# Performance work log

Hardware: AMD Instinct MI355X
Metric: run time of the kernel (lower is better)

The kernel has to match this reference:

```python
import jax, jax.numpy as jnp
import numpy as np

BLOCK_NUM = 64
B, M, K, N = 4, 4096, 4096, 4096  # batch, rows, in_features, out_features


def setup_inputs() -> dict:
    key = jax.random.key(0)
    k1, k2 = jax.random.split(key)
    x = jax.random.normal(k1, (B, M, K), dtype=jnp.float32)
    weight = jax.random.normal(k2, (K, N), dtype=jnp.float32) * 0.02
    return {"x": x, "weight": weight}


def reference(x, weight):
    # Block-local matmul: output block (i, j) = A_block(i, j) @ W_block(i, j).
    # No cross-block reduction: each (i, j) output block depends on exactly one
    # A block and one W block. Vectorized as a single einsum over all blocks.
    b, m, k = x.shape
    k2, n = weight.shape
    Bn = BLOCK_NUM
    r, c, o = m // Bn, k // Bn, n // Bn  # per-block rows / contract / cols
    A = x.reshape(b, Bn, r, Bn, c)        # [b, i, r, j, c]
    W = weight.reshape(Bn, c, Bn, o)      # [i, c, j, o] (rows split by i, cols by j)
    out = jnp.einsum('birjc,icjo->birjo', A, W)
    return out.reshape(b, m, n)
```

## Files before the change

### kernel.cpp

```cpp
#include <hip/hip_runtime.h>
#include <hip/hip_bf16.h>


typedef short bf16x8 __attribute__((ext_vector_type(8)));
typedef float f32x4 __attribute__((ext_vector_type(4)));

__device__ __forceinline__ unsigned short f2bf(float f) {
    union { float f; unsigned int u; } v; v.f = f;
    unsigned int u = v.u;
    u += 0x7fffu + ((u >> 16) & 1u);
    return (unsigned short)(u >> 16);
}

__global__ __launch_bounds__(256, 4) void block_matmul_kernel(
    const float* __restrict__ x, const float* __restrict__ w,
    float* __restrict__ out) {
    __shared__ unsigned short As[64 * 64];
    __shared__ unsigned short Ws[64 * 64];

    const int nwg   = 4 * 64 * 64;
    const int chunk = nwg >> 3;
    int orig = blockIdx.x;
    int wg   = (orig & 7) * chunk + (orig >> 3);

    int b  = wg & 3;
    int ij = wg >> 2;
    int i  = ij >> 6;
    int j  = ij & 63;

    const float* Ab = x   + ((size_t)b * 4096 + (size_t)i * 64) * 4096 + (size_t)j * 64;
    const float* Wb = w   + ((size_t)i * 64) * 4096 + (size_t)j * 64;
    float*       Ob = out + ((size_t)b * 4096 + (size_t)i * 64) * 4096 + (size_t)j * 64;

    const int t = threadIdx.x;

    #pragma unroll
    for (int it = 0; it < 4; ++it) {
        int idx = it * 256 + t;
        int m   = idx >> 4;
        int k4  = (idx & 15) << 2;
        float4 v = *reinterpret_cast<const float4*>(Ab + (size_t)m * 4096 + k4);
        unsigned long long pk =
            (unsigned long long)f2bf(v.x)        |
            ((unsigned long long)f2bf(v.y) << 16) |
            ((unsigned long long)f2bf(v.z) << 32) |
            ((unsigned long long)f2bf(v.w) << 48);
        int addr = m * 128 + ((k4 * 2) ^ ((m & 7) << 4));
        *reinterpret_cast<unsigned long long*>(reinterpret_cast<char*>(As) + addr) = pk;
    }

    {
        int n  = t & 63;
        int kq = (t >> 6) << 2;
        #pragma unroll
        for (int it = 0; it < 4; ++it) {
            int kb = it * 16 + kq;
            float f0 = Wb[(size_t)(kb + 0) * 4096 + n];
            float f1 = Wb[(size_t)(kb + 1) * 4096 + n];
            float f2 = Wb[(size_t)(kb + 2) * 4096 + n];
            float f3 = Wb[(size_t)(kb + 3) * 4096 + n];
            unsigned long long pk =
                (unsigned long long)f2bf(f0)        |
                ((unsigned long long)f2bf(f1) << 16) |
                ((unsigned long long)f2bf(f2) << 32) |
                ((unsigned long long)f2bf(f3) << 48);
            int addr = n * 128 + ((kb * 2) ^ ((n & 7) << 4));
            *reinterpret_cast<unsigned long long*>(reinterpret_cast<char*>(Ws) + addr) = pk;
        }
    }

    __syncthreads();

    const int l  = t & 63;
    const int wv = t >> 6;
    const int lr = l & 15;
    const int lk = l >> 4;

    f32x4 acc[4] = {{0.f,0.f,0.f,0.f},{0.f,0.f,0.f,0.f},
                    {0.f,0.f,0.f,0.f},{0.f,0.f,0.f,0.f}};

    #pragma unroll
    for (int kt = 0; kt < 2; ++kt) {
        int kbyte = kt * 64 + lk * 16;
        int am = wv * 16 + lr;
        bf16x8 af = *reinterpret_cast<const bf16x8*>(
            reinterpret_cast<const char*>(As) + am * 128 + (kbyte ^ ((am & 7) << 4)));
        #pragma unroll
        for (int nt = 0; nt < 4; ++nt) {
            int bn = nt * 16 + lr;
            bf16x8 bfr = *reinterpret_cast<const bf16x8*>(
                reinterpret_cast<const char*>(Ws) + bn * 128 + (kbyte ^ ((bn & 7) << 4)));
            acc[nt] = __builtin_amdgcn_mfma_f32_16x16x32_bf16(af, bfr, acc[nt], 0, 0, 0);
        }
    }

    #pragma unroll
    for (int nt = 0; nt < 4; ++nt) {
        #pragma unroll
        for (int r = 0; r < 4; ++r) {
            int orow = wv * 16 + lk * 4 + r;
            int ocol = nt * 16 + lr;
            Ob[(size_t)orow * 4096 + ocol] = acc[nt][r];
        }
    }
}

extern "C" void kernel_launch(void* const* d_in, const int* in_sizes, int n_in,
                              void* d_out, int out_size, void* d_ws, size_t ws_size,
                              hipStream_t stream) {
    const float* x = (const float*)d_in[0];
    const float* w = (const float*)d_in[1];
    float* out = (float*)d_out;

    dim3 grid(4 * 64 * 64);
    dim3 block(256);
    block_matmul_kernel<<<grid, block, 0, stream>>>(x, w, out);
}
```

Before: 143.5 us.

## Reuse weight block across batch and pipeline A loads via global_load_lds

Each workgroup now handles one (i,j) block for all four batches: it loads and converts the weight block once, then streams the fp32 A tiles for each batch straight into LDS with global_load_lds, double-buffered with explicit vmcnt waits so the next batch's load overlaps the current MFMA and store. The grid shrinks by a factor of four. This removes the repeated weight loads and the register round trip for A, at the cost of more LDS per workgroup and hand-tuned vmcnt counts that must match the outstanding loads and stores exactly.

New measurement: 148.6 us. 1.04x slower.

```diff
diff --git a/kernel.cpp b/kernel.cpp
--- a/kernel.cpp
+++ b/kernel.cpp
@@ -12,97 +12,127 @@
     return (unsigned short)(u >> 16);
 }
 
+__device__ __forceinline__ bf16x8 pack8(float4 a, float4 b) {
+    bf16x8 r;
+    r[0] = (short)f2bf(a.x); r[1] = (short)f2bf(a.y);
+    r[2] = (short)f2bf(a.z); r[3] = (short)f2bf(a.w);
+    r[4] = (short)f2bf(b.x); r[5] = (short)f2bf(b.y);
+    r[6] = (short)f2bf(b.z); r[7] = (short)f2bf(b.w);
+    return r;
+}
+
+#define BBYTES 67108864ull
+#define BELEMS 16777216ull
+
+#define WAITV(N) do { asm volatile("s_waitcnt vmcnt(" #N ")" ::: "memory"); \
+                      __builtin_amdgcn_sched_barrier(0); } while (0)
+
 __global__ __launch_bounds__(256, 4) void block_matmul_kernel(
     const float* __restrict__ x, const float* __restrict__ w,
     float* __restrict__ out) {
-    __shared__ unsigned short As[64 * 64];
-    __shared__ unsigned short Ws[64 * 64];
+    __shared__ char smem[40960];
 
-    const int nwg   = 4 * 64 * 64;
-    const int chunk = nwg >> 3;
+    const int t   = threadIdx.x;
+    const int l   = t & 63;
+    const int wv  = t >> 6;
+    const int lr  = l & 15;
+    const int lhi = l >> 4;
+
     int orig = blockIdx.x;
-    int wg   = (orig & 7) * chunk + (orig >> 3);
+    int wg   = (orig & 7) * 512 + (orig >> 3);
+    int i = wg >> 6;
+    int j = wg & 63;
 
-    int b  = wg & 3;
-    int ij = wg >> 2;
-    int i  = ij >> 6;
-    int j  = ij & 63;
+    const size_t rowbase = (size_t)i * 64;
+    const size_t colbase = (size_t)j * 64;
 
-    const float* Ab = x   + ((size_t)b * 4096 + (size_t)i * 64) * 4096 + (size_t)j * 64;
-    const float* Wb = w   + ((size_t)i * 64) * 4096 + (size_t)j * 64;
-    float*       Ob = out + ((size_t)b * 4096 + (size_t)i * 64) * 4096 + (size_t)j * 64;
-
-    const int t = threadIdx.x;
-
+    const float* Wb = w + rowbase * 4096 + colbase;
+    const int wn = t & 63;
+    const int cg = t >> 6;
+    float wreg[16];
+    #pragma unroll
+    for (int it = 0; it < 4; ++it)
+        #pragma unroll
+        for (int r = 0; r < 4; ++r)
+            wreg[it * 4 + r] = Wb[(size_t)(cg * 16 + it * 4 + r) * 4096 + wn];
     #pragma unroll
     for (int it = 0; it < 4; ++it) {
-        int idx = it * 256 + t;
-        int m   = idx >> 4;
-        int k4  = (idx & 15) << 2;
-        float4 v = *reinterpret_cast<const float4*>(Ab + (size_t)m * 4096 + k4);
+        int cc = (cg * 16 + it * 4) * 2;
         unsigned long long pk =
-            (unsigned long long)f2bf(v.x)        |
-            ((unsigned long long)f2bf(v.y) << 16) |
-            ((unsigned long long)f2bf(v.z) << 32) |
-            ((unsigned long long)f2bf(v.w) << 48);
-        int addr = m * 128 + ((k4 * 2) ^ ((m & 7) << 4));
-        *reinterpret_cast<unsigned long long*>(reinterpret_cast<char*>(As) + addr) = pk;
+            (unsigned long long)f2bf(wreg[it * 4 + 0])         |
+            ((unsigned long long)f2bf(wreg[it * 4 + 1]) << 16) |
+            ((unsigned long long)f2bf(wreg[it * 4 + 2]) << 32) |
+            ((unsigned long long)f2bf(wreg[it * 4 + 3]) << 48);
+        *reinterpret_cast<unsigned long long*>(
+            smem + wn * 128 + (cc ^ ((wn & 7) << 4))) = pk;
+    }
+    __syncthreads();
+
+    const char* Axbase = (const char*)x +
+        ((rowbase + wv * 16) * 4096 + colbase) * 4;
+    const int c16 = (l & 15) * 16;
+
+#define DMA(b_, p_) {                                                         \
+    _Pragma("unroll") for (int s = 0; s < 4; ++s) {                           \
+        int rl   = s * 4 + lhi;                                               \
+        int csrc = c16 ^ ((rl & 7) << 4);                                     \
+        const char* gp = Axbase + (size_t)(b_) * BBYTES +                     \
+                         (size_t)rl * 16384 + csrc;                           \
+        char* lp = smem + 8192 + (p_) * 16384 + wv * 4096 + s * 1024;         \
+        __builtin_amdgcn_global_load_lds(                                     \
+            (const __attribute__((address_space(1))) void*)gp,                \
+            (__attribute__((address_space(3))) void*)lp, 16, 0, 0);           \
+    } }
+
+    char* Alane = smem + 8192 + wv * 4096 + lr * 256;
+    const int fsw = (lr & 7) << 4;
+
+    DMA(0, 0);
+    DMA(1, 1);
+
+#define BATCH(b_, p_, NW, NEXT, HASNEXT) {                                    \
+    WAITV(NW);                                                                \
+    const char* Ab = Alane + (p_) * 16384;                                    \
+    float4 f00 = *reinterpret_cast<const float4*>(                            \
+        Ab + ((lhi * 32) ^ fsw));                                             \
+    float4 f01 = *reinterpret_cast<const float4*>(                            \
+        Ab + ((lhi * 32 + 16) ^ fsw));                                        \
+    float4 f10 = *reinterpret_cast<const float4*>(                            \
+        Ab + ((128 + lhi * 32) ^ fsw));                                       \
+    float4 f11 = *reinterpret_cast<const float4*>(                            \
+        Ab + ((128 + lhi * 32 + 16) ^ fsw));                                  \
+    bf16x8 af0 = pack8(f00, f01);                                             \
+    bf16x8 af1 = pack8(f10, f11);                                             \
+    __builtin_amdgcn_sched_barrier(0);                                        \
+    if (HASNEXT) DMA(NEXT, p_);                                               \
+    f32x4 acc[4];                                                             \
+    _Pragma("unroll") for (int nt = 0; nt < 4; ++nt)                          \
+        acc[nt] = (f32x4){0.f, 0.f, 0.f, 0.f};                                \
+    _Pragma("unroll") for (int nt = 0; nt < 4; ++nt) {                        \
+        int bn = nt * 16 + lr;                                                \
+        bf16x8 w0 = *reinterpret_cast<const bf16x8*>(                         \
+            smem + bn * 128 + ((lhi * 16) ^ ((bn & 7) << 4)));                \
+        acc[nt] = __builtin_amdgcn_mfma_f32_16x16x32_bf16(                    \
+            af0, w0, acc[nt], 0, 0, 0);                                       \
+    }                                                                         \
+    _Pragma("unroll") for (int nt = 0; nt < 4; ++nt) {                        \
+        int bn = nt * 16 + lr;                                                \
+        bf16x8 w1 = *reinterpret_cast<const bf16x8*>(                         \
+            smem + bn * 128 + ((64 + lhi * 16) ^ ((bn & 7) << 4)));           \
+        acc[nt] = __builtin_amdgcn_mfma_f32_16x16x32_bf16(                    \
+            af1, w1, acc[nt], 0, 0, 0);                                       \
+    }                                                                         \
+    float* Ob = out + (size_t)(b_) * BELEMS +                                 \
+                (rowbase + wv * 16) * 4096 + colbase;                         \
+    _Pragma("unroll") for (int nt = 0; nt < 4; ++nt)                          \
+    _Pragma("unroll") for (int r = 0; r < 4; ++r)                             \
+        Ob[(size_t)(lhi * 4 + r) * 4096 + nt * 16 + lr] = acc[nt][r];         \
     }
 
-    {
-        int n  = t & 63;
-        int kq = (t >> 6) << 2;
-        #pragma unroll
-        for (int it = 0; it < 4; ++it) {
-            int kb = it * 16 + kq;
-            float f0 = Wb[(size_t)(kb + 0) * 4096 + n];
-            float f1 = Wb[(size_t)(kb + 1) * 4096 + n];
-            float f2 = Wb[(size_t)(kb + 2) * 4096 + n];
-            float f3 = Wb[(size_t)(kb + 3) * 4096 + n];
-            unsigned long long pk =
-                (unsigned long long)f2bf(f0)        |
-                ((unsigned long long)f2bf(f1) << 16) |
-                ((unsigned long long)f2bf(f2) << 32) |
-                ((unsigned long long)f2bf(f3) << 48);
-            int addr = n * 128 + ((kb * 2) ^ ((n & 7) << 4));
-            *reinterpret_cast<unsigned long long*>(reinterpret_cast<char*>(Ws) + addr) = pk;
-        }
-    }
-
-    __syncthreads();
-
-    const int l  = t & 63;
-    const int wv = t >> 6;
-    const int lr = l & 15;
-    const int lk = l >> 4;
-
-    f32x4 acc[4] = {{0.f,0.f,0.f,0.f},{0.f,0.f,0.f,0.f},
-                    {0.f,0.f,0.f,0.f},{0.f,0.f,0.f,0.f}};
-
-    #pragma unroll
-    for (int kt = 0; kt < 2; ++kt) {
-        int kbyte = kt * 64 + lk * 16;
-        int am = wv * 16 + lr;
-        bf16x8 af = *reinterpret_cast<const bf16x8*>(
-            reinterpret_cast<const char*>(As) + am * 128 + (kbyte ^ ((am & 7) << 4)));
-        #pragma unroll
-        for (int nt = 0; nt < 4; ++nt) {
-            int bn = nt * 16 + lr;
-            bf16x8 bfr = *reinterpret_cast<const bf16x8*>(
-                reinterpret_cast<const char*>(Ws) + bn * 128 + (kbyte ^ ((bn & 7) << 4)));
-            acc[nt] = __builtin_amdgcn_mfma_f32_16x16x32_bf16(af, bfr, acc[nt], 0, 0, 0);
-        }
-    }
-
-    #pragma unroll
-    for (int nt = 0; nt < 4; ++nt) {
-        #pragma unroll
-        for (int r = 0; r < 4; ++r) {
-            int orow = wv * 16 + lk * 4 + r;
-            int ocol = nt * 16 + lr;
-            Ob[(size_t)orow * 4096 + ocol] = acc[nt][r];
-        }
-    }
+    BATCH(0, 0, 4,  2, 1);
+    BATCH(1, 1, 20, 3, 1);
+    BATCH(2, 0, 36, 0, 0);
+    BATCH(3, 1, 32, 0, 0);
 }
 
 extern "C" void kernel_launch(void* const* d_in, const int* in_sizes, int n_in,
@@ -112,7 +142,7 @@
     const float* w = (const float*)d_in[1];
     float* out = (float*)d_out;
 
-    dim3 grid(4 * 64 * 64);
+    dim3 grid(4096);
     dim3 block(256);
     block_matmul_kernel<<<grid, block, 0, stream>>>(x, w, out);
 }
```

## Process four adjacent blocks per workgroup with wide coalesced loads and LDS-staged stores

Applied to the files above, without the earlier changes.

Each workgroup now handles a 64x256 strip (four neighbouring j blocks) instead of one 64x64 block, cutting the grid from 16384 to 4096 workgroups. All global loads are issued up front into registers as full-row 1 KB coalesced float4 reads before the bf16 conversion. The output is staged through LDS with a swizzle so each row is written with wide float4 stores instead of scattered scalar stores. The trade-off is 64 KB of LDS, higher register use, and a lower occupancy target of 2 blocks per SIMD instead of 4, which may reduce latency hiding for this memory-bound kernel.

New measurement: 128.3 us. -10.6%, faster.

```diff
diff --git a/kernel.cpp b/kernel.cpp
--- a/kernel.cpp
+++ b/kernel.cpp
@@ -12,96 +12,135 @@
     return (unsigned short)(u >> 16);
 }
 
-__global__ __launch_bounds__(256, 4) void block_matmul_kernel(
+__device__ __forceinline__ unsigned long long pack4(float4 v) {
+    return  (unsigned long long)f2bf(v.x)        |
+           ((unsigned long long)f2bf(v.y) << 16) |
+           ((unsigned long long)f2bf(v.z) << 32) |
+           ((unsigned long long)f2bf(v.w) << 48);
+}
+
+__device__ __forceinline__ unsigned long long pack4s(float a, float b,
+                                                     float c, float d) {
+    return  (unsigned long long)f2bf(a)        |
+           ((unsigned long long)f2bf(b) << 16) |
+           ((unsigned long long)f2bf(c) << 32) |
+           ((unsigned long long)f2bf(d) << 48);
+}
+
+#define BELEMS 16777216ull
+
+#define FENCE() asm volatile("s_waitcnt lgkmcnt(0)" ::: "memory")
+
+__global__ __launch_bounds__(256, 2) void block_matmul_kernel(
     const float* __restrict__ x, const float* __restrict__ w,
     float* __restrict__ out) {
-    __shared__ unsigned short As[64 * 64];
-    __shared__ unsigned short Ws[64 * 64];
+    __shared__ char smem[65536];
 
-    const int nwg   = 4 * 64 * 64;
-    const int chunk = nwg >> 3;
+    const int t   = threadIdx.x;
+    const int l   = t & 63;
+    const int wv  = t >> 6;
+    const int lr  = l & 15;
+    const int lhi = l >> 4;
+
     int orig = blockIdx.x;
-    int wg   = (orig & 7) * chunk + (orig >> 3);
+    int wg   = (orig & 7) * 512 + (orig >> 3);
+    int b  = wg >> 10;
+    int i  = (wg >> 4) & 63;
+    int q8 = wg & 15;
 
-    int b  = wg & 3;
-    int ij = wg >> 2;
-    int i  = ij >> 6;
-    int j  = ij & 63;
+    const size_t rowbase = (size_t)i * 64;
+    const size_t colbase = (size_t)q8 * 256;
 
-    const float* Ab = x   + ((size_t)b * 4096 + (size_t)i * 64) * 4096 + (size_t)j * 64;
-    const float* Wb = w   + ((size_t)i * 64) * 4096 + (size_t)j * 64;
-    float*       Ob = out + ((size_t)b * 4096 + (size_t)i * 64) * 4096 + (size_t)j * 64;
+    const float* Ab = x + (size_t)b * BELEMS + rowbase * 4096 + colbase;
+    const float* Wb = w + rowbase * 4096 + colbase;
+    float*       Ob = out + (size_t)b * BELEMS + rowbase * 4096 + colbase;
 
-    const int t = threadIdx.x;
+    float4 areg[16];
+    {
+        const float* p = Ab + (size_t)(wv * 16) * 4096 + l * 4;
+        #pragma unroll
+        for (int s = 0; s < 16; ++s)
+            areg[s] = *reinterpret_cast<const float4*>(p + (size_t)s * 4096);
+    }
+    float wreg[16][4];
+    {
+        const float* p = Wb + (size_t)(wv * 16) * 4096 + l;
+        #pragma unroll
+        for (int s = 0; s < 16; ++s)
+            #pragma unroll
+            for (int h = 0; h < 4; ++h)
+                wreg[s][h] = p[(size_t)s * 4096 + h * 64];
+    }
 
     #pragma unroll
-    for (int it = 0; it < 4; ++it) {
-        int idx = it * 256 + t;
-        int m   = idx >> 4;
-        int k4  = (idx & 15) << 2;
-        float4 v = *reinterpret_cast<const float4*>(Ab + (size_t)m * 4096 + k4);
-        unsigned long long pk =
-            (unsigned long long)f2bf(v.x)        |
-            ((unsigned long long)f2bf(v.y) << 16) |
-            ((unsigned long long)f2bf(v.z) << 32) |
-            ((unsigned long long)f2bf(v.w) << 48);
-        int addr = m * 128 + ((k4 * 2) ^ ((m & 7) << 4));
-        *reinterpret_cast<unsigned long long*>(reinterpret_cast<char*>(As) + addr) = pk;
+    for (int s = 0; s < 16; ++s) {
+        int m = wv * 16 + s;
+        *reinterpret_cast<unsigned long long*>(
+            smem + m * 512 + ((l * 8) ^ ((m & 7) << 4))) = pack4(areg[s]);
     }
-
-    {
-        int n  = t & 63;
-        int kq = (t >> 6) << 2;
+    #pragma unroll
+    for (int g = 0; g < 4; ++g) {
+        int c0 = wv * 16 + g * 4;
         #pragma unroll
-        for (int it = 0; it < 4; ++it) {
-            int kb = it * 16 + kq;
-            float f0 = Wb[(size_t)(kb + 0) * 4096 + n];
-            float f1 = Wb[(size_t)(kb + 1) * 4096 + n];
-            float f2 = Wb[(size_t)(kb + 2) * 4096 + n];
-            float f3 = Wb[(size_t)(kb + 3) * 4096 + n];
-            unsigned long long pk =
-                (unsigned long long)f2bf(f0)        |
-                ((unsigned long long)f2bf(f1) << 16) |
-                ((unsigned long long)f2bf(f2) << 32) |
-                ((unsigned long long)f2bf(f3) << 48);
-            int addr = n * 128 + ((kb * 2) ^ ((n & 7) << 4));
-            *reinterpret_cast<unsigned long long*>(reinterpret_cast<char*>(Ws) + addr) = pk;
+        for (int h = 0; h < 4; ++h) {
+            int n = l + h * 64;
+            unsigned long long pk = pack4s(wreg[g*4+0][h], wreg[g*4+1][h],
+                                           wreg[g*4+2][h], wreg[g*4+3][h]);
+            *reinterpret_cast<unsigned long long*>(
+                smem + 32768 + n * 128 + ((c0 * 2) ^ ((n & 7) << 4))) = pk;
         }
     }
 
     __syncthreads();
 
-    const int l  = t & 63;
-    const int wv = t >> 6;
-    const int lr = l & 15;
-    const int lk = l >> 4;
+    f32x4 acc[4][4];
+    #pragma unroll
+    for (int a = 0; a < 4; ++a)
+        #pragma unroll
+        for (int z = 0; z < 4; ++z) acc[a][z] = (f32x4){0.f,0.f,0.f,0.f};
 
-    f32x4 acc[4] = {{0.f,0.f,0.f,0.f},{0.f,0.f,0.f,0.f},
-                    {0.f,0.f,0.f,0.f},{0.f,0.f,0.f,0.f}};
-
+    const int m = wv * 16 + lr;
     #pragma unroll
-    for (int kt = 0; kt < 2; ++kt) {
-        int kbyte = kt * 64 + lk * 16;
-        int am = wv * 16 + lr;
-        bf16x8 af = *reinterpret_cast<const bf16x8*>(
-            reinterpret_cast<const char*>(As) + am * 128 + (kbyte ^ ((am & 7) << 4)));
+    for (int jloc = 0; jloc < 4; ++jloc) {
         #pragma unroll
-        for (int nt = 0; nt < 4; ++nt) {
-            int bn = nt * 16 + lr;
-            bf16x8 bfr = *reinterpret_cast<const bf16x8*>(
-                reinterpret_cast<const char*>(Ws) + bn * 128 + (kbyte ^ ((bn & 7) << 4)));
-            acc[nt] = __builtin_amdgcn_mfma_f32_16x16x32_bf16(af, bfr, acc[nt], 0, 0, 0);
+        for (int kt = 0; kt < 2; ++kt) {
+            bf16x8 af = *reinterpret_cast<const bf16x8*>(
+                smem + m * 512 +
+                ((jloc * 128 + kt * 64 + lhi * 16) ^ ((m & 7) << 4)));
+            #pragma unroll
+            for (int nt = 0; nt < 4; ++nt) {
+                int n = jloc * 64 + nt * 16 + lr;
+                bf16x8 bfr = *reinterpret_cast<const bf16x8*>(
+                    smem + 32768 + n * 128 +
+                    ((kt * 64 + lhi * 16) ^ ((n & 7) << 4)));
+                acc[jloc][nt] = __builtin_amdgcn_mfma_f32_16x16x32_bf16(
+                    af, bfr, acc[jloc][nt], 0, 0, 0);
+            }
         }
     }
 
+    __syncthreads();
+
     #pragma unroll
-    for (int nt = 0; nt < 4; ++nt) {
+    for (int jloc = 0; jloc < 4; ++jloc)
         #pragma unroll
-        for (int r = 0; r < 4; ++r) {
-            int orow = wv * 16 + lk * 4 + r;
-            int ocol = nt * 16 + lr;
-            Ob[(size_t)orow * 4096 + ocol] = acc[nt][r];
-        }
+        for (int nt = 0; nt < 4; ++nt)
+            #pragma unroll
+            for (int r = 0; r < 4; ++r) {
+                int mr  = wv * 16 + lhi * 4 + r;
+                int col = jloc * 64 + nt * 16 + lr;
+                *reinterpret_cast<float*>(
+                    smem + mr * 1024 + ((col * 4) ^ ((mr & 7) << 4)))
+                    = acc[jloc][nt][r];
+            }
+    FENCE();
+
+    #pragma unroll
+    for (int s = 0; s < 16; ++s) {
+        int mr = wv * 16 + s;
+        f32x4 v = *reinterpret_cast<const f32x4*>(
+            smem + mr * 1024 + ((l * 16) ^ ((mr & 7) << 4)));
+        *reinterpret_cast<f32x4*>(Ob + (size_t)mr * 4096 + l * 4) = v;
     }
 }
 
@@ -112,7 +151,7 @@
     const float* w = (const float*)d_in[1];
     float* out = (float*)d_out;
 
-    dim3 grid(4 * 64 * 64);
+    dim3 grid(4096);
     dim3 block(256);
     block_matmul_kernel<<<grid, block, 0, stream>>>(x, w, out);
 }
```
